# Kernel optimization log

Hardware: AMD Instinct MI355X
Metric: run time of the kernel (lower is better)

Reference implementation:

```python
import jax, jax.numpy as jnp
import numpy as np

HIDDEN = 768
NUM_HEADS = 12
HEAD_DIM = HIDDEN // NUM_HEADS
WINDOW = 128
NEG = -1e30  # stand-in for -inf that is safe under autodiff


def setup_inputs() -> dict:
    key = jax.random.key(0)
    ks = jax.random.split(key, 12)
    B, S = 2, 2048
    hidden = jax.random.normal(ks[0], (B, S, HIDDEN), dtype=jnp.float32)
    attention_mask = jnp.ones((B, S), dtype=jnp.int32)
    global_mask = jax.random.randint(ks[1], (B, S), 0, 2, dtype=jnp.int32)
    def lin(kw, kb):
        W = jax.random.normal(kw, (HIDDEN, HIDDEN), dtype=jnp.float32) * 0.02
        b = jax.random.normal(kb, (HIDDEN,), dtype=jnp.float32) * 0.02
        return W, b
    Wq, bq = lin(ks[2], ks[3])
    Wk, bk = lin(ks[4], ks[5])
    Wv, bv = lin(ks[6], ks[7])
    Wo, bo = lin(ks[8], ks[9])
    return {"hidden": hidden, "attention_mask": attention_mask, "global_mask": global_mask,
            "Wq": Wq, "bq": bq, "Wk": Wk, "bk": bk, "Wv": Wv, "bv": bv, "Wo": Wo, "bo": bo}


def _attend(hidden, attention_mask, global_mask, Wq, bq, Wk, bk, Wv, bv, Wo, bo):
    B, S, H = hidden.shape
    def proj(W, b):
        # (B,S,H) -> (B,nh,S,hd); nn.Linear computes x @ W.T + b
        return (hidden @ W.T + b).reshape(B, S, NUM_HEADS, HEAD_DIM).transpose(0, 2, 1, 3)
    q, k, v = proj(Wq, bq), proj(Wk, bk), proj(Wv, bv)
    scale = jnp.asarray(np.sqrt(HEAD_DIM), dtype=hidden.dtype)
    scores = jnp.einsum('bhqd,bhkd->bhqk', q, k) / scale  # (B,nh,S,S)
    # sliding window mask: |i-j| <= WINDOW
    idx = jnp.arange(S)
    window = (jnp.abs(idx[:, None] - idx[None, :]) <= WINDOW)  # (S,S)
    g = global_mask.astype(bool)
    combined = window[None] | g[:, :, None] | g[:, None, :]     # (B,S,S)
    combined = combined & attention_mask.astype(bool)[:, None, :]  # pad mask on keys
    scores = jnp.where(combined[:, None, :, :], scores, NEG)
    attn = jax.nn.softmax(scores, axis=-1)
    # torch code zeroes NaN rows (fully masked); replicate safely
    attn = jnp.where(jnp.isnan(attn), 0.0, attn)
    out = jnp.einsum('bhqk,bhkd->bhqd', attn, v)  # (B,nh,S,hd)
    out = out.transpose(0, 2, 1, 3).reshape(B, S, H)
    return out @ Wo.T + bo


def reference(hidden, attention_mask, global_mask, Wq, bq, Wk, bk, Wv, bv, Wo, bo):
    return _attend(hidden, attention_mask, global_mask, Wq, bq, Wk, bk, Wv, bv, Wo, bo)
```

## Files before the change

### kernel.cpp

```cpp
#include <hip/hip_runtime.h>
#include <math.h>

#define S_LEN 2048
#define HID   768
#define NH    12
#define HD    64
#define WIN   128
#define NEGV  (-1e30f)
#define QSCALE 0.1803368801111204f

typedef __attribute__((ext_vector_type(8))) short short8v;
typedef __attribute__((ext_vector_type(4))) float float4v;
typedef unsigned short u16;

__device__ __forceinline__ u16 f2bf(float f) {
    union { float f; unsigned int u; } c; c.f = f;
    unsigned int u = c.u + 0x7FFFu + ((c.u >> 16) & 1u);
    return (u16)(u >> 16);
}

__device__ __forceinline__ short8v cvt8(float4 a, float4 b) {
    short8v t;
    t[0]=(short)f2bf(a.x); t[1]=(short)f2bf(a.y); t[2]=(short)f2bf(a.z); t[3]=(short)f2bf(a.w);
    t[4]=(short)f2bf(b.x); t[5]=(short)f2bf(b.y); t[6]=(short)f2bf(b.z); t[7]=(short)f2bf(b.w);
    return t;
}

__device__ __forceinline__ unsigned int pk2bf(float a, float b) {
    unsigned int r;
    asm("v_cvt_pk_bf16_f32 %0, %1, %2" : "=v"(r) : "v"(a), "v"(b));
    return r;
}

__device__ __forceinline__ float exp2_fast(float x) {
    float r;
    asm("v_exp_f32 %0, %1" : "=v"(r) : "v"(x));
    return r;
}

__device__ __forceinline__ void gload_lds16(const void* g, void* l) {
    __builtin_amdgcn_global_load_lds(
        (const __attribute__((address_space(1))) unsigned int*)g,
        (__attribute__((address_space(3))) unsigned int*)l, 16, 0, 0);
}

__global__ __launch_bounds__(256) void convert_inputs(
    const float* __restrict__ hidden, const float* __restrict__ Wq,
    const float* __restrict__ Wk, const float* __restrict__ Wv,
    const float* __restrict__ Wo, u16* __restrict__ hbf, u16* __restrict__ w4)
{
    const int y = blockIdx.y;
    const float* src; u16* dst; int n; float scale = 1.f;
    if (y == 0) { src = hidden; dst = hbf; n = 4096*HID; }
    else {
        src = (y==1) ? Wq : (y==2) ? Wk : (y==3) ? Wv : Wo;
        dst = w4 + (size_t)(y-1)*HID*HID;
        n = HID*HID;
        if (y == 1) scale = QSCALE;
    }
    const int idx = (blockIdx.x*256 + threadIdx.x) * 8;
    if (idx >= n) return;
    float4 f0 = *(const float4*)(src + idx);
    float4 f1 = *(const float4*)(src + idx + 4);
    f0.x*=scale; f0.y*=scale; f0.z*=scale; f0.w*=scale;
    f1.x*=scale; f1.y*=scale; f1.z*=scale; f1.w*=scale;
    *(short8v*)(dst + idx) = cvt8(f0, f1);
}

__global__ __launch_bounds__(256) void gemm_mfma(
    const u16* __restrict__ A, const u16* __restrict__ W4,
    const float* __restrict__ bA, const float* __restrict__ bB,
    const float* __restrict__ bC, u16* __restrict__ obf,
    u16* __restrict__ ovt, float* __restrict__ of32, int mode)
{
    __shared__ __align__(16) u16 As[128*32];
    __shared__ __align__(16) u16 Bs[128*32];

    const int tid = threadIdx.x;
    const int w = tid >> 6, l = tid & 63;
    const int lx = l & 15, lg = l >> 4;
    const int wr = w >> 1, wc = w & 1;
    const int m0 = blockIdx.x * 128, n0 = blockIdx.y * 128;
    const int z = (mode == 0) ? blockIdx.z : 3;
    const float* bias = (mode == 1) ? bA : (z == 0 ? bA : (z == 1 ? bB : bC));
    const float bscale = (mode == 0 && z == 0) ? QSCALE : 1.0f;
    const u16* Wp = W4 + (size_t)z * (HID*HID);

    float4v acc[4][4];
    const float4v fz = {0.f,0.f,0.f,0.f};
    #pragma unroll
    for (int i = 0; i < 4; i++)
        #pragma unroll
        for (int j = 0; j < 4; j++) acc[i][j] = fz;

    for (int kt = 0; kt < HID/32; kt++) {
        const int k0 = kt * 32;
        __syncthreads();
        #pragma unroll
        for (int rnd = 0; rnd < 2; rnd++) {
            const int ch  = rnd*256 + w*64 + l;
            const int row = ch >> 2, kc = ch & 3;
            gload_lds16(A  + (size_t)(m0+row)*HID + k0 + kc*8,
                        As + (size_t)(rnd*256 + w*64)*8);
            gload_lds16(Wp + (size_t)(n0+row)*HID + k0 + kc*8,
                        Bs + (size_t)(rnd*256 + w*64)*8);
        }
        __syncthreads();
        short8v af[4], bfr[4];
        #pragma unroll
        for (int i = 0; i < 4; i++) {
            af[i]  = *(const short8v*)(As + (wr*64 + i*16 + lx)*32 + lg*8);
            bfr[i] = *(const short8v*)(Bs + (wc*64 + i*16 + lx)*32 + lg*8);
        }
        #pragma unroll
        for (int i = 0; i < 4; i++)
            #pragma unroll
            for (int j = 0; j < 4; j++)
                acc[i][j] = __builtin_amdgcn_mfma_f32_16x16x32_bf16(af[i], bfr[j], acc[i][j], 0, 0, 0);
    }

    #pragma unroll
    for (int j = 0; j < 4; j++) {
        const int col = n0 + wc*64 + j*16 + lx;
        const float bval = bias[col] * bscale;
        const int hh = col >> 6, d = col & 63;
        #pragma unroll
        for (int i = 0; i < 4; i++) {
            const int rbase = m0 + wr*64 + i*16 + lg*4;
            const int bb = rbase >> 11, s = rbase & 2047;
            const float v0 = acc[i][j][0] + bval;
            const float v1 = acc[i][j][1] + bval;
            const float v2 = acc[i][j][2] + bval;
            const float v3 = acc[i][j][3] + bval;
            if (mode == 1) {
                of32[(size_t)(rbase+0)*HID + col] = v0;
                of32[(size_t)(rbase+1)*HID + col] = v1;
                of32[(size_t)(rbase+2)*HID + col] = v2;
                of32[(size_t)(rbase+3)*HID + col] = v3;
            } else if (z == 2) {
                uint2 ow; ow.x = pk2bf(v0, v1); ow.y = pk2bf(v2, v3);
                *(uint2*)&ovt[(((size_t)bb*NH + hh)*HD + d)*S_LEN + s] = ow;
            } else {
                u16* base = obf + (size_t)z * ((size_t)2*S_LEN*HID);
                base[(((size_t)bb*NH + hh)*S_LEN + s+0)*HD + d] = f2bf(v0);
                base[(((size_t)bb*NH + hh)*S_LEN + s+1)*HD + d] = f2bf(v1);
                base[(((size_t)bb*NH + hh)*S_LEN + s+2)*HD + d] = f2bf(v2);
                base[(((size_t)bb*NH + hh)*S_LEN + s+3)*HD + d] = f2bf(v3);
            }
        }
    }
}

__global__ __launch_bounds__(256) void attn_mfma(
    const u16* __restrict__ Q, const u16* __restrict__ K,
    const u16* __restrict__ Vt, const int* __restrict__ amask,
    const int* __restrict__ gmask, u16* __restrict__ AO)
{
    __shared__ __align__(16) u16 KsA[64*64], VsA[64*64];
    __shared__ __align__(16) u16 KsB[64*64], VsB[64*64];
    __shared__ __align__(16) u16 Ps[4*16*64];
    __shared__ __align__(16) float fA[64];
    __shared__ __align__(16) float fB[64];

    const int tid = threadIdx.x;
    const int w  = tid >> 6;
    const int l  = tid & 63;
    const int lx = l & 15;
    const int lg = l >> 4;

    const int bid = blockIdx.x;
    const int swz = (bid & 7) * 96 + (bid >> 3);
    const int q0 = (swz & 31) * 64;
    const int hb = swz >> 5;
    const int h  = hb % NH;
    const int b  = hb / NH;
    const size_t bh = ((size_t)b*NH + h) * S_LEN;

    const int q_glob = q0 + w*16 + lx;

    short8v aq[2];
    {
        const u16* qp = Q + (bh + q_glob)*HD + lg*8;
        aq[0] = *(const short8v*)(qp);
        aq[1] = *(const short8v*)(qp + 32);
    }
    const int gq = gmask[(size_t)b*S_LEN + q_glob];
    const float* fP = gq ? fA : fB;

    float m_i = NEGV, l_i = 0.f;
    float4v o_acc[4];
    const float4v fzv = {0.f, 0.f, 0.f, 0.f};
    #pragma unroll
    for (int db = 0; db < 4; db++) o_acc[db] = fzv;

    const int str = tid >> 2;
    const int stc = tid & 3;
    const int rb  = str * 128;
    const int sw  = (str & 7) << 4;
    const u16* Kbase = K + bh * HD;
    const u16* Vbase = Vt + (size_t)(b*NH + h) * HD * S_LEN;
    const int psw = (lx & 7) << 4;

    uint4 rk0, rk1, rv0, rv1;
    int ram = 0, rgk = 0;

#define STAGE_REGS(KT) do {                                                   \
    const int kk0_ = (KT) * 64;                                               \
    const u16* kp_ = Kbase + (size_t)(kk0_ + str)*HD + stc*16;                \
    rk0 = *(const uint4*)(kp_); rk1 = *(const uint4*)(kp_ + 8);               \
    const u16* vp_ = Vbase + (size_t)str*S_LEN + kk0_ + stc*16;               \
    rv0 = *(const uint4*)(vp_); rv1 = *(const uint4*)(vp_ + 8);               \
    if (tid < 64) {                                                           \
        ram = amask[(size_t)b*S_LEN + kk0_ + tid];                            \
        rgk = gmask[(size_t)b*S_LEN + kk0_ + tid];                            \
    }                                                                         \
} while(0)

#define WRITE_LDS(KS, VS) do {                                                \
    *(uint4*)((char*)(KS) + rb + ((stc*32)      ^ sw)) = rk0;                 \
    *(uint4*)((char*)(KS) + rb + ((stc*32 + 16) ^ sw)) = rk1;                 \
    *(uint4*)((char*)(VS) + rb + ((stc*32)      ^ sw)) = rv0;                 \
    *(uint4*)((char*)(VS) + rb + ((stc*32 + 16) ^ sw)) = rv1;                 \
    if (tid < 64) {                                                           \
        fA[tid] = ram ? 0.f : NEGV;                                           \
        fB[tid] = (ram && rgk) ? 0.f : NEGV;                                  \
    }                                                                         \
} while(0)

#define COMPUTE(KS, VS, K0) do {                                              \
    float4v sacc[4];                                                          \
    _Pragma("unroll")                                                         \
    for (int kb = 0; kb < 4; kb++) sacc[kb] = fzv;                            \
    _Pragma("unroll")                                                         \
    for (int kb = 0; kb < 4; kb++) {                                          \
        const int key_ = kb*16 + lx;                                          \
        const int ksw_ = (key_ & 7) << 4;                                     \
        _Pragma("unroll")                                                     \
        for (int ks = 0; ks < 2; ks++) {                                      \
            short8v bk_ = *(const short8v*)((char*)(KS) + key_*128 +          \
                                            ((16*lg + 64*ks) ^ ksw_));        \
            sacc[kb] = __builtin_amdgcn_mfma_f32_16x16x32_bf16(bk_, aq[ks],   \
                                                          sacc[kb], 0, 0, 0); \
        }                                                                     \
    }                                                                         \
    float sv[4][4];                                                           \
    const int adq_ = ((K0) > q0) ? ((K0) - q0) : (q0 - (K0));                 \
    if (adq_ <= 64) {                                                         \
        _Pragma("unroll")                                                     \
        for (int kb = 0; kb < 4; kb++) {                                      \
            float4 fa4 = *(const float4*)&fA[kb*16 + lg*4];                   \
            sv[kb][0] = sacc[kb][0] + fa4.x;                                  \
            sv[kb][1] = sacc[kb][1] + fa4.y;                                  \
            sv[kb][2] = sacc[kb][2] + fa4.z;                                  \
            sv[kb][3] = sacc[kb][3] + fa4.w;                                  \
        }                                                                     \
    } else if (adq_ >= 192) {                                                 \
        _Pragma("unroll")                                                     \
        for (int kb = 0; kb < 4; kb++) {                                      \
            float4 fp4 = *(const float4*)&fP[kb*16 + lg*4];                   \
            sv[kb][0] = sacc[kb][0] + fp4.x;                                  \
            sv[kb][1] = sacc[kb][1] + fp4.y;                                  \
            sv[kb][2] = sacc[kb][2] + fp4.z;                                  \
            sv[kb][3] = sacc[kb][3] + fp4.w;                                  \
        }                                                                     \
    } else {                                                                  \
        _Pragma("unroll")                                                     \
        for (int kb = 0; kb < 4; kb++) {                                      \
            float4 fa4 = *(const float4*)&fA[kb*16 + lg*4];                   \
            float4 fb4 = *(const float4*)&fB[kb*16 + lg*4];                   \
            const int e_ = q_glob - ((K0) + kb*16 + lg*4);                    \
            _Pragma("unroll")                                                 \
            for (int r = 0; r < 4; r++) {                                     \
                int dd_ = e_ - r; dd_ = dd_ < 0 ? -dd_ : dd_;                 \
                const bool wing_ = (dd_ <= WIN) || gq;                        \
                const float fa_ = (&fa4.x)[r], fb_ = (&fb4.x)[r];             \
                sv[kb][r] = sacc[kb][r] + (wing_ ? fa_ : fb_);                \
            }                                                                 \
        }                                                                     \
    }                                                                         \
    float mloc;                                                               \
    {                                                                         \
        float t0 = fmaxf(fmaxf(sv[0][0], sv[0][1]), fmaxf(sv[0][2], sv[0][3]));\
        float t1 = fmaxf(fmaxf(sv[1][0], sv[1][1]), fmaxf(sv[1][2], sv[1][3]));\
        float t2 = fmaxf(fmaxf(sv[2][0], sv[2][1]), fmaxf(sv[2][2], sv[2][3]));\
        float t3 = fmaxf(fmaxf(sv[3][0], sv[3][1]), fmaxf(sv[3][2], sv[3][3]));\
        mloc = fmaxf(fmaxf(t0, t1), fmaxf(t2, t3));                           \
    }                                                                         \
    mloc = fmaxf(mloc, __shfl_xor(mloc, 16));                                 \
    mloc = fmaxf(mloc, __shfl_xor(mloc, 32));                                 \
    if (__any(mloc > m_i + 8.0f)) {                                           \
        const float mnew_ = fmaxf(m_i, mloc);                                 \
        const float sc_ = exp2_fast(m_i - mnew_);                             \
        l_i *= sc_;                                                           \
        _Pragma("unroll")                                                     \
        for (int db = 0; db < 4; db++)                                        \
            _Pragma("unroll")                                                 \
            for (int r = 0; r < 4; r++) o_acc[db][r] *= sc_;                  \
        m_i = mnew_;                                                          \
    }                                                                         \
    float p[4][4];                                                            \
    float lsum = 0.f;                                                         \
    _Pragma("unroll")                                                         \
    for (int kb = 0; kb < 4; kb++)                                            \
        _Pragma("unroll")                                                     \
        for (int r = 0; r < 4; r++) {                                         \
            p[kb][r] = exp2_fast(sv[kb][r] - m_i);                            \
            lsum += p[kb][r];                                                 \
        }                                                                     \
    lsum += __shfl_xor(lsum, 16);                                             \
    lsum += __shfl_xor(lsum, 32);                                             \
    l_i += lsum;                                                              \
    _Pragma("unroll")                                                         \
    for (int kb = 0; kb < 4; kb++) {                                          \
        uint2 pw;                                                             \
        pw.x = pk2bf(p[kb][0], p[kb][1]);                                     \
        pw.y = pk2bf(p[kb][2], p[kb][3]);                                     \
        *(uint2*)((char*)Ps + w*2048 + lx*128 + ((kb*32 + lg*8) ^ psw)) = pw; \
    }                                                                         \
    _Pragma("unroll")                                                         \
    for (int ks = 0; ks < 2; ks++) {                                          \
        short8v pa_ = *(const short8v*)((char*)Ps + w*2048 + lx*128 +         \
                                        ((16*lg + 64*ks) ^ psw));             \
        _Pragma("unroll")                                                     \
        for (int db = 0; db < 4; db++) {                                      \
            const int drow_ = db*16 + lx;                                     \
            short8v bv_ = *(const short8v*)((char*)(VS) + drow_*128 +         \
                                    ((16*lg + 64*ks) ^ ((drow_ & 7) << 4)));  \
            o_acc[db] = __builtin_amdgcn_mfma_f32_16x16x32_bf16(bv_, pa_,     \
                                                          o_acc[db], 0, 0, 0);\
        }                                                                     \
    }                                                                         \
} while(0)

    STAGE_REGS(0);
    WRITE_LDS(KsA, VsA);
    __syncthreads();

    for (int kt = 0; kt < S_LEN/64; kt += 2) {
        STAGE_REGS(kt+1);
        COMPUTE(KsA, VsA, kt*64);
        __syncthreads();
        WRITE_LDS(KsB, VsB);
        __syncthreads();
        {
            const int kn = (kt+2 < S_LEN/64) ? (kt+2) : (S_LEN/64 - 1);
            STAGE_REGS(kn);
        }
        COMPUTE(KsB, VsB, (kt+1)*64);
        __syncthreads();
        WRITE_LDS(KsA, VsA);
        __syncthreads();
    }

#undef STAGE_REGS
#undef WRITE_LDS
#undef COMPUTE

    {
        const float inv = 1.f / l_i;
        u16* op = AO + ((size_t)b*S_LEN + q_glob)*HID + h*HD + lg*4;
        #pragma unroll
        for (int db = 0; db < 4; db++) {
            uint2 ow;
            ow.x = pk2bf(o_acc[db][0]*inv, o_acc[db][1]*inv);
            ow.y = pk2bf(o_acc[db][2]*inv, o_acc[db][3]*inv);
            *(uint2*)(op + db*16) = ow;
        }
    }
}

extern "C" void kernel_launch(void* const* d_in, const int* in_sizes, int n_in,
                              void* d_out, int out_size, void* d_ws, size_t ws_size,
                              hipStream_t stream)
{
    const float* hidden = (const float*)d_in[0];
    const int*   amask  = (const int*)d_in[1];
    const int*   gmask  = (const int*)d_in[2];
    const float* Wq = (const float*)d_in[3];
    const float* bq = (const float*)d_in[4];
    const float* Wk = (const float*)d_in[5];
    const float* bk = (const float*)d_in[6];
    const float* Wv = (const float*)d_in[7];
    const float* bv = (const float*)d_in[8];
    const float* Wo = (const float*)d_in[9];
    const float* bo = (const float*)d_in[10];
    float* out = (float*)d_out;

    char* ws = (char*)d_ws;
    const size_t NTOK = (size_t)2 * S_LEN * HID;
    u16* hbf   = (u16*)(ws);
    u16* w4    = (u16*)(ws + 6291456);
    u16* qkvbf = (u16*)(ws + 11010048);
    u16* vtbf  = (u16*)(ws + 29884416);
    u16* aobf  = (u16*)(ws + 36175872);

    convert_inputs<<<dim3(1536, 5), 256, 0, stream>>>(hidden, Wq, Wk, Wv, Wo, hbf, w4);

    gemm_mfma<<<dim3(32, 6, 3), 256, 0, stream>>>(hbf, w4, bq, bk, bv, qkvbf, vtbf, nullptr, 0);

    u16* Qbf = qkvbf;
    u16* Kbf = qkvbf + NTOK;

    attn_mfma<<<dim3(768), 256, 0, stream>>>(Qbf, Kbf, vtbf, amask, gmask, aobf);

    gemm_mfma<<<dim3(32, 6), 256, 0, stream>>>(aobf, w4, bo, nullptr, nullptr, nullptr, nullptr, out, 1);
}
```

Measured before the change: 107.9 us.

## Double-buffer mask arrays, drop per-tile barrier, fold mask into MFMA accumulator init

Double-buffers the per-key mask bias arrays so each K/V tile has its own copy, then removes one of the two __syncthreads per tile. Compute on buffer A now overlaps the writes into buffer B. The mask bias is loaded into the MFMA accumulator before the QK^T MFMAs, which removes the separate add pass and the sv array. s_setprio is raised around the MFMA sections, and the max and sum reductions are rebalanced into shallower trees. The risk is that removing a barrier opens a race between WRITE_LDS into the other buffer and waves still reading it from the previous iteration.

```diff
diff --git a/kernel.cpp b/kernel.cpp
--- a/kernel.cpp
+++ b/kernel.cpp
@@ -159,8 +159,8 @@
     __shared__ __align__(16) u16 KsA[64*64], VsA[64*64];
     __shared__ __align__(16) u16 KsB[64*64], VsB[64*64];
     __shared__ __align__(16) u16 Ps[4*16*64];
-    __shared__ __align__(16) float fA[64];
-    __shared__ __align__(16) float fB[64];
+    __shared__ __align__(16) float fAa[64], fBa[64];
+    __shared__ __align__(16) float fAb[64], fBb[64];
 
     const int tid = threadIdx.x;
     const int w  = tid >> 6;
@@ -185,7 +185,8 @@
         aq[1] = *(const short8v*)(qp + 32);
     }
     const int gq = gmask[(size_t)b*S_LEN + q_glob];
-    const float* fP = gq ? fA : fB;
+    const float* fPa = gq ? fAa : fBa;
+    const float* fPb = gq ? fAb : fBb;
 
     float m_i = NEGV, l_i = 0.f;
     float4v o_acc[4];
@@ -216,21 +217,50 @@
     }                                                                         \
 } while(0)
 
-#define WRITE_LDS(KS, VS) do {                                                \
+#define WRITE_LDS(KS, VS, FA, FB) do {                                        \
     *(uint4*)((char*)(KS) + rb + ((stc*32)      ^ sw)) = rk0;                 \
     *(uint4*)((char*)(KS) + rb + ((stc*32 + 16) ^ sw)) = rk1;                 \
     *(uint4*)((char*)(VS) + rb + ((stc*32)      ^ sw)) = rv0;                 \
     *(uint4*)((char*)(VS) + rb + ((stc*32 + 16) ^ sw)) = rv1;                 \
     if (tid < 64) {                                                           \
-        fA[tid] = ram ? 0.f : NEGV;                                           \
-        fB[tid] = (ram && rgk) ? 0.f : NEGV;                                  \
+        (FA)[tid] = ram ? 0.f : NEGV;                                         \
+        (FB)[tid] = (ram && rgk) ? 0.f : NEGV;                                \
     }                                                                         \
 } while(0)
 
-#define COMPUTE(KS, VS, K0) do {                                              \
+#define COMPUTE(KS, VS, FA, FB, FP, K0) do {                                  \
+                           \
     float4v sacc[4];                                                          \
-    _Pragma("unroll")                                                         \
-    for (int kb = 0; kb < 4; kb++) sacc[kb] = fzv;                            \
+    const int adq_ = ((K0) > q0) ? ((K0) - q0) : (q0 - (K0));                 \
+    if (adq_ <= 64) {                                                         \
+        _Pragma("unroll")                                                     \
+        for (int kb = 0; kb < 4; kb++) {                                      \
+            float4 fa4 = *(const float4*)&(FA)[kb*16 + lg*4];                 \
+            sacc[kb][0]=fa4.x; sacc[kb][1]=fa4.y;                             \
+            sacc[kb][2]=fa4.z; sacc[kb][3]=fa4.w;                             \
+        }                                                                     \
+    } else if (adq_ >= 192) {                                                 \
+        _Pragma("unroll")                                                     \
+        for (int kb = 0; kb < 4; kb++) {                                      \
+            float4 fp4 = *(const float4*)&(FP)[kb*16 + lg*4];                 \
+            sacc[kb][0]=fp4.x; sacc[kb][1]=fp4.y;                             \
+            sacc[kb][2]=fp4.z; sacc[kb][3]=fp4.w;                             \
+        }                                                                     \
+    } else {                                                                  \
+        _Pragma("unroll")                                                     \
+        for (int kb = 0; kb < 4; kb++) {                                      \
+            float4 fa4 = *(const float4*)&(FA)[kb*16 + lg*4];                 \
+            float4 fb4 = *(const float4*)&(FB)[kb*16 + lg*4];                 \
+            const int e_ = q_glob - ((K0) + kb*16 + lg*4);                    \
+            _Pragma("unroll")                                                 \
+            for (int r = 0; r < 4; r++) {                                     \
+                int dd_ = e_ - r; dd_ = dd_ < 0 ? -dd_ : dd_;                 \
+                const bool wing_ = (dd_ <= WIN) || gq;                        \
+                sacc[kb][r] = wing_ ? (&fa4.x)[r] : (&fb4.x)[r];              \
+            }                                                                 \
+        }                                                                     \
+    }                                                                         \
+    __builtin_amdgcn_s_setprio(1);                                            \
     _Pragma("unroll")                                                         \
     for (int kb = 0; kb < 4; kb++) {                                          \
         const int key_ = kb*16 + lx;                                          \
@@ -243,48 +273,17 @@
                                                           sacc[kb], 0, 0, 0); \
         }                                                                     \
     }                                                                         \
-    float sv[4][4];                                                           \
-    const int adq_ = ((K0) > q0) ? ((K0) - q0) : (q0 - (K0));                 \
-    if (adq_ <= 64) {                                                         \
-        _Pragma("unroll")                                                     \
-        for (int kb = 0; kb < 4; kb++) {                                      \
-            float4 fa4 = *(const float4*)&fA[kb*16 + lg*4];                   \
-            sv[kb][0] = sacc[kb][0] + fa4.x;                                  \
-            sv[kb][1] = sacc[kb][1] + fa4.y;                                  \
-            sv[kb][2] = sacc[kb][2] + fa4.z;                                  \
-            sv[kb][3] = sacc[kb][3] + fa4.w;                                  \
-        }                                                                     \
-    } else if (adq_ >= 192) {                                                 \
-        _Pragma("unroll")                                                     \
-        for (int kb = 0; kb < 4; kb++) {                                      \
-            float4 fp4 = *(const float4*)&fP[kb*16 + lg*4];                   \
-            sv[kb][0] = sacc[kb][0] + fp4.x;                                  \
-            sv[kb][1] = sacc[kb][1] + fp4.y;                                  \
-            sv[kb][2] = sacc[kb][2] + fp4.z;                                  \
-            sv[kb][3] = sacc[kb][3] + fp4.w;                                  \
-        }                                                                     \
-    } else {                                                                  \
-        _Pragma("unroll")                                                     \
-        for (int kb = 0; kb < 4; kb++) {                                      \
-            float4 fa4 = *(const float4*)&fA[kb*16 + lg*4];                   \
-            float4 fb4 = *(const float4*)&fB[kb*16 + lg*4];                   \
-            const int e_ = q_glob - ((K0) + kb*16 + lg*4);                    \
-            _Pragma("unroll")                                                 \
-            for (int r = 0; r < 4; r++) {                                     \
-                int dd_ = e_ - r; dd_ = dd_ < 0 ? -dd_ : dd_;                 \
-                const bool wing_ = (dd_ <= WIN) || gq;                        \
-                const float fa_ = (&fa4.x)[r], fb_ = (&fb4.x)[r];             \
-                sv[kb][r] = sacc[kb][r] + (wing_ ? fa_ : fb_);                \
-            }                                                                 \
-        }                                                                     \
-    }                                                                         \
+    __builtin_amdgcn_s_setprio(0);                                            \
+                                \
     float mloc;                                                               \
     {                                                                         \
-        float t0 = fmaxf(fmaxf(sv[0][0], sv[0][1]), fmaxf(sv[0][2], sv[0][3]));\
-        float t1 = fmaxf(fmaxf(sv[1][0], sv[1][1]), fmaxf(sv[1][2], sv[1][3]));\
-        float t2 = fmaxf(fmaxf(sv[2][0], sv[2][1]), fmaxf(sv[2][2], sv[2][3]));\
-        float t3 = fmaxf(fmaxf(sv[3][0], sv[3][1]), fmaxf(sv[3][2], sv[3][3]));\
-        mloc = fmaxf(fmaxf(t0, t1), fmaxf(t2, t3));                           \
+        float t0 = fmaxf(fmaxf(sacc[0][0], sacc[0][1]), sacc[0][2]);          \
+        float t1 = fmaxf(fmaxf(sacc[0][3], sacc[1][0]), sacc[1][1]);          \
+        float t2 = fmaxf(fmaxf(sacc[1][2], sacc[1][3]), sacc[2][0]);          \
+        float t3 = fmaxf(fmaxf(sacc[2][1], sacc[2][2]), sacc[2][3]);          \
+        float t4 = fmaxf(fmaxf(sacc[3][0], sacc[3][1]), sacc[3][2]);          \
+        mloc = fmaxf(fmaxf(fmaxf(t0, t1), t2),                                \
+                     fmaxf(fmaxf(t3, t4), sacc[3][3]));                       \
     }                                                                         \
     mloc = fmaxf(mloc, __shfl_xor(mloc, 16));                                 \
     mloc = fmaxf(mloc, __shfl_xor(mloc, 32));                                 \
@@ -299,17 +298,21 @@
         m_i = mnew_;                                                          \
     }                                                                         \
     float p[4][4];                                                            \
-    float lsum = 0.f;                                                         \
     _Pragma("unroll")                                                         \
     for (int kb = 0; kb < 4; kb++)                                            \
         _Pragma("unroll")                                                     \
-        for (int r = 0; r < 4; r++) {                                         \
-            p[kb][r] = exp2_fast(sv[kb][r] - m_i);                            \
-            lsum += p[kb][r];                                                 \
-        }                                                                     \
-    lsum += __shfl_xor(lsum, 16);                                             \
-    lsum += __shfl_xor(lsum, 32);                                             \
-    l_i += lsum;                                                              \
+        for (int r = 0; r < 4; r++)                                           \
+            p[kb][r] = exp2_fast(sacc[kb][r] - m_i);                          \
+    {                                                                         \
+        float s0 = (p[0][0]+p[0][1]) + (p[0][2]+p[0][3]);                     \
+        float s1 = (p[1][0]+p[1][1]) + (p[1][2]+p[1][3]);                     \
+        float s2 = (p[2][0]+p[2][1]) + (p[2][2]+p[2][3]);                     \
+        float s3 = (p[3][0]+p[3][1]) + (p[3][2]+p[3][3]);                     \
+        float lsum = (s0+s1) + (s2+s3);                                       \
+        lsum += __shfl_xor(lsum, 16);                                         \
+        lsum += __shfl_xor(lsum, 32);                                         \
+        l_i += lsum;                                                          \
+    }                                                                         \
     _Pragma("unroll")                                                         \
     for (int kb = 0; kb < 4; kb++) {                                          \
         uint2 pw;                                                             \
@@ -317,6 +320,7 @@
         pw.y = pk2bf(p[kb][2], p[kb][3]);                                     \
         *(uint2*)((char*)Ps + w*2048 + lx*128 + ((kb*32 + lg*8) ^ psw)) = pw; \
     }                                                                         \
+    __builtin_amdgcn_s_setprio(1);                                            \
     _Pragma("unroll")                                                         \
     for (int ks = 0; ks < 2; ks++) {                                          \
         short8v pa_ = *(const short8v*)((char*)Ps + w*2048 + lx*128 +         \
@@ -330,25 +334,24 @@
                                                           o_acc[db], 0, 0, 0);\
         }                                                                     \
     }                                                                         \
+    __builtin_amdgcn_s_setprio(0);                                            \
 } while(0)
 
     STAGE_REGS(0);
-    WRITE_LDS(KsA, VsA);
+    WRITE_LDS(KsA, VsA, fAa, fBa);
     __syncthreads();
 
     for (int kt = 0; kt < S_LEN/64; kt += 2) {
         STAGE_REGS(kt+1);
-        COMPUTE(KsA, VsA, kt*64);
-        __syncthreads();
-        WRITE_LDS(KsB, VsB);
+        COMPUTE(KsA, VsA, fAa, fBa, fPa, kt*64);
+        WRITE_LDS(KsB, VsB, fAb, fBb);
         __syncthreads();
         {
             const int kn = (kt+2 < S_LEN/64) ? (kt+2) : (S_LEN/64 - 1);
             STAGE_REGS(kn);
         }
-        COMPUTE(KsB, VsB, (kt+1)*64);
-        __syncthreads();
-        WRITE_LDS(KsA, VsA);
+        COMPUTE(KsB, VsB, fAb, fBb, fPb, (kt+1)*64);
+        WRITE_LDS(KsA, VsA, fAa, fBa);
         __syncthreads();
     }
 
```

Result: no change. 106.1 us (-1.7%).
